# Kernel optimization log

Measured on AMD Instinct MI355X. Metric: run time of the kernel, lower is better.

## Reference

```python
import jax, jax.numpy as jnp
import numpy as np

N_NODES = 10000
N_EDGES = 160000
IN_DIM = 256
HEADS = 8
C0 = 32   # per-head out channels, layer 0 (256 // 8)
C1 = 32   # per-head out channels, layer 1 (= output_dim)
RANK = 8
LORA_SCALE = 32.0 / 8      # alpha / rank
ATT_RANK = 4               # rank // 2
ATT_SCALE = 32.0 / 4       # alpha / (rank // 2)
NEG_SLOPE = 0.2


def _gat_layer(x, src, dst, W, A, B, att_s, att_d, As, Bs, Ad, Bd, concat):
    """One LoRAGATConv layer (eval mode, dropout=0)."""
    N = x.shape[0]
    H, C = att_s.shape
    # LoRA-adapted projection: base + B(A x) * scaling -> [N, H, C]
    xp = (x @ W.T + ((x @ A.T) @ B.T) * LORA_SCALE).reshape(N, H, C)

    def att_score(base, Aa, Ba):
        # per-head base dot product + LoRA(out_channels -> 1) path -> [N, H]
        return jnp.einsum('nhc,hc->nh', xp, base) + ((xp @ Aa.T) @ Ba.T)[..., 0] * ATT_SCALE

    s_src = att_score(att_s, As, Bs)  # applied to x_i (destination), per original code
    s_dst = att_score(att_d, Ad, Bd)  # applied to x_j (source), per original code

    alpha = s_src[dst] + s_dst[src]              # [E, H]
    alpha = jax.nn.leaky_relu(alpha, NEG_SLOPE)
    # segment softmax over destination nodes (every node has a self-loop)
    m = jax.ops.segment_max(alpha, dst, num_segments=N)
    e = jnp.exp(alpha - m[dst])
    den = jax.ops.segment_sum(e, dst, num_segments=N)
    a = e / den[dst]                             # [E, H]

    msg = xp[src] * a[:, :, None]                # [E, H, C]
    out = jax.ops.segment_sum(msg, dst, num_segments=N)  # [N, H, C]
    return out.reshape(N, H * C) if concat else out.mean(axis=1)


def _forward(x, edge_index,
             W0, A0, B0, att_src0, att_dst0, Asrc0, Bsrc0, Adst0, Bdst0,
             W1, A1, B1, att_src1, att_dst1, Asrc1, Bsrc1, Adst1, Bdst1):
    N = x.shape[0]
    loops = jnp.arange(N, dtype=edge_index.dtype)
    ei = jnp.concatenate([edge_index, jnp.stack([loops, loops])], axis=1)
    src, dst = ei[0], ei[1]
    h = _gat_layer(x, src, dst, W0, A0, B0, att_src0, att_dst0, Asrc0, Bsrc0, Adst0, Bdst0, concat=True)
    h = jax.nn.elu(h)
    out = _gat_layer(h, src, dst, W1, A1, B1, att_src1, att_dst1, Asrc1, Bsrc1, Adst1, Bdst1, concat=False)
    return out


def setup_inputs() -> dict:
    key = jax.random.key(0)
    ks = jax.random.split(key, 24)
    s = 0.05
    inp = {
        'x': jax.random.normal(ks[0], (N_NODES, IN_DIM), dtype=jnp.float32),
        'edge_index': jax.random.randint(ks[1], (2, N_EDGES), 0, N_NODES, dtype=jnp.int64),
    }
    # layer 0: in 256 -> heads*C0 = 256
    inp['W0'] = jax.random.normal(ks[2], (HEADS * C0, IN_DIM), dtype=jnp.float32) * s
    inp['A0'] = jax.random.normal(ks[3], (RANK, IN_DIM), dtype=jnp.float32) * s
    inp['B0'] = jax.random.normal(ks[4], (HEADS * C0, RANK), dtype=jnp.float32) * s
    inp['att_src0'] = jax.random.normal(ks[5], (HEADS, C0), dtype=jnp.float32) * s
    inp['att_dst0'] = jax.random.normal(ks[6], (HEADS, C0), dtype=jnp.float32) * s
    inp['Asrc0'] = jax.random.normal(ks[7], (ATT_RANK, C0), dtype=jnp.float32) * s
    inp['Bsrc0'] = jax.random.normal(ks[8], (1, ATT_RANK), dtype=jnp.float32) * s
    inp['Adst0'] = jax.random.normal(ks[9], (ATT_RANK, C0), dtype=jnp.float32) * s
    inp['Bdst0'] = jax.random.normal(ks[10], (1, ATT_RANK), dtype=jnp.float32) * s
    # layer 1: in heads*C0 = 256 -> heads*C1 = 256 (head-averaged -> 32)
    D1 = HEADS * C0
    inp['W1'] = jax.random.normal(ks[11], (HEADS * C1, D1), dtype=jnp.float32) * s
    inp['A1'] = jax.random.normal(ks[12], (RANK, D1), dtype=jnp.float32) * s
    inp['B1'] = jax.random.normal(ks[13], (HEADS * C1, RANK), dtype=jnp.float32) * s
    inp['att_src1'] = jax.random.normal(ks[14], (HEADS, C1), dtype=jnp.float32) * s
    inp['att_dst1'] = jax.random.normal(ks[15], (HEADS, C1), dtype=jnp.float32) * s
    inp['Asrc1'] = jax.random.normal(ks[16], (ATT_RANK, C1), dtype=jnp.float32) * s
    inp['Bsrc1'] = jax.random.normal(ks[17], (1, ATT_RANK), dtype=jnp.float32) * s
    inp['Adst1'] = jax.random.normal(ks[18], (ATT_RANK, C1), dtype=jnp.float32) * s
    inp['Bdst1'] = jax.random.normal(ks[19], (1, ATT_RANK), dtype=jnp.float32) * s
    return inp


def reference(x, edge_index,
              W0, A0, B0, att_src0, att_dst0, Asrc0, Bsrc0, Adst0, Bdst0,
              W1, A1, B1, att_src1, att_dst1, Asrc1, Bsrc1, Adst1, Bdst1):
    return _forward(x, edge_index,
                    W0, A0, B0, att_src0, att_dst0, Asrc0, Bsrc0, Adst0, Bdst0,
                    W1, A1, B1, att_src1, att_dst1, Asrc1, Bsrc1, Adst1, Bdst1)
```

## Files before the change

### kernel.cpp

```cpp
#include <hip/hip_runtime.h>

#define LORA_SCALE 4.0f
#define ATT_SCALE 8.0f
#define NEG_SLOPE 0.2f
#define ELLW 64

typedef __attribute__((ext_vector_type(8))) short bf16x8;
typedef __attribute__((ext_vector_type(4))) float f32x4;
typedef unsigned short ushort_t;
typedef unsigned int uint_t;

__device__ inline ushort_t f2bf(float f) {
    uint_t u = __float_as_uint(f);
    u += 0x7fff + ((u >> 16) & 1);
    return (ushort_t)(u >> 16);
}
__device__ inline float bf2f(ushort_t h) {
    return __uint_as_float(((uint_t)h) << 16);
}
__device__ inline void split_bf(float f, ushort_t& h, ushort_t& l) {
    h = f2bf(f);
    l = f2bf(f - bf2f(h));
}

__global__ void prep_all(const float* __restrict__ W0, const float* __restrict__ A0,
                         const float* __restrict__ B0,
                         const float* __restrict__ att_s0, const float* __restrict__ att_d0,
                         const float* __restrict__ As0, const float* __restrict__ Bs0,
                         const float* __restrict__ Ad0, const float* __restrict__ Bd0,
                         const float* __restrict__ W1, const float* __restrict__ A1,
                         const float* __restrict__ B1,
                         const float* __restrict__ att_s1, const float* __restrict__ att_d1,
                         const float* __restrict__ As1, const float* __restrict__ Bs1,
                         const float* __restrict__ Ad1, const float* __restrict__ Bd1,
                         ushort_t* __restrict__ whi0, ushort_t* __restrict__ wlo0,
                         ushort_t* __restrict__ whi1, ushort_t* __restrict__ wlo1,
                         float* __restrict__ effS0, float* __restrict__ effD0,
                         float* __restrict__ effS1, float* __restrict__ effD1,
                         const float* __restrict__ x, ushort_t* __restrict__ xhi,
                         ushort_t* __restrict__ xlo,
                         const int* __restrict__ ei, int E_real, int E_total,
                         int* __restrict__ cnt, int* __restrict__ ell, int N)
{
    int b = blockIdx.x;
    int t = threadIdx.x;
    if (b < 512) {
        int layer = b >> 8;
        int i = (b & 255) * 256 + t;
        const float* W = layer ? W1 : W0;
        const float* A = layer ? A1 : A0;
        const float* B = layer ? B1 : B0;
        int r = i >> 8, c = i & 255;
        float acc = W[i];
        #pragma unroll
        for (int k = 0; k < 8; k++) acc += LORA_SCALE * B[r * 8 + k] * A[k * 256 + c];
        ushort_t h, l;
        split_bf(acc, h, l);
        if (layer) { whi1[i] = h; wlo1[i] = l; }
        else       { whi0[i] = h; wlo0[i] = l; }
        if (i < 256) {
            int c2 = i & 31;
            const float* as_ = layer ? att_s1 : att_s0;
            const float* ad_ = layer ? att_d1 : att_d0;
            const float* As = layer ? As1 : As0;
            const float* Bs = layer ? Bs1 : Bs0;
            const float* Ad = layer ? Ad1 : Ad0;
            const float* Bd = layer ? Bd1 : Bd0;
            float es = as_[i], ed = ad_[i];
            #pragma unroll
            for (int k = 0; k < 4; k++) {
                es += ATT_SCALE * Bs[k] * As[k * 32 + c2];
                ed += ATT_SCALE * Bd[k] * Ad[k * 32 + c2];
            }
            if (layer) { effS1[i] = es; effD1[i] = ed; }
            else       { effS0[i] = es; effD0[i] = ed; }
        }
        return;
    }
    int cb = b - 512;
    int convB = (N * 32 + 255) / 256;
    if (cb < convB) {
        int i = cb * 256 + t;
        if (i >= N * 32) return;
        float4 v0 = *(const float4*)(x + i * 8);
        float4 v1 = *(const float4*)(x + i * 8 + 4);
        ushort4 h0, l0, h1, l1;
        split_bf(v0.x, h0.x, l0.x);
        split_bf(v0.y, h0.y, l0.y);
        split_bf(v0.z, h0.z, l0.z);
        split_bf(v0.w, h0.w, l0.w);
        split_bf(v1.x, h1.x, l1.x);
        split_bf(v1.y, h1.y, l1.y);
        split_bf(v1.z, h1.z, l1.z);
        split_bf(v1.w, h1.w, l1.w);
        *(ushort4*)(xhi + i * 8) = h0;
        *(ushort4*)(xhi + i * 8 + 4) = h1;
        *(ushort4*)(xlo + i * 8) = l0;
        *(ushort4*)(xlo + i * 8 + 4) = l1;
        return;
    }
    int e = (cb - convB) * 256 + t;
    if (e >= E_total) return;
    int s, d;
    if (e < E_real) { s = ei[e]; d = ei[E_real + e]; }
    else            { s = d = e - E_real; }
    int pos = atomicAdd(&cnt[d], 1);
    if (pos < ELLW) ell[d * ELLW + pos] = s;
}

__global__ __launch_bounds__(512) void gemm_fused(
    const ushort_t* __restrict__ Ahi, const ushort_t* __restrict__ Alo,
    const ushort_t* __restrict__ Bhi, const ushort_t* __restrict__ Blo,
    const float* __restrict__ effS, const float* __restrict__ effD,
    ushort_t* __restrict__ Cb, float* __restrict__ ssrc, float* __restrict__ sdst, int M)
{
    __shared__ ushort_t sBh[16384];
    __shared__ ushort_t sBl[16384];
    const int K = 256;
    int tid = threadIdx.x;
    int n0 = blockIdx.x * 64;

    const ushort_t* srcH = Bhi + (size_t)n0 * K;
    const ushort_t* srcL = Blo + (size_t)n0 * K;
    #pragma unroll
    for (int c = 0; c < 4; c++) {
        int g  = c * 512 + tid;
        int rr = g >> 5;
        int ch = g & 31;
        int kblk = ch >> 2, quad = ch & 3;
        int tt = rr >> 4, l16r = rr & 15;
        int dst = (((tt * 8 + kblk) * 4 + quad) * 16 + l16r) * 8;
        *(bf16x8*)&sBh[dst] = *(const bf16x8*)(srcH + rr * K + ch * 8);
        *(bf16x8*)&sBl[dst] = *(const bf16x8*)(srcL + rr * K + ch * 8);
    }
    __syncthreads();

    int w = tid >> 6;
    int lane = tid & 63;
    int quad = lane >> 4;
    int l16 = lane & 15;
    int m0 = blockIdx.y * 128 + w * 16;
    int mr = m0 + l16; if (mr >= M) mr = M - 1;

    const ushort_t* ah = Ahi + mr * K + quad * 8;
    const ushort_t* al = Alo + mr * K + quad * 8;

    f32x4 acc[4] = {};
    #pragma unroll
    for (int kb = 0; kb < 8; kb++) {
        bf16x8 a_hi = *(const bf16x8*)(ah + kb * 32);
        bf16x8 a_lo = *(const bf16x8*)(al + kb * 32);
        #pragma unroll
        for (int t = 0; t < 4; t++) {
            int off = (((t * 8 + kb) * 4 + quad) * 16 + l16) * 8;
            bf16x8 b_hi = *(const bf16x8*)&sBh[off];
            bf16x8 b_lo = *(const bf16x8*)&sBl[off];
            acc[t] = __builtin_amdgcn_mfma_f32_16x16x32_bf16(a_hi, b_hi, acc[t], 0, 0, 0);
            acc[t] = __builtin_amdgcn_mfma_f32_16x16x32_bf16(a_hi, b_lo, acc[t], 0, 0, 0);
            acc[t] = __builtin_amdgcn_mfma_f32_16x16x32_bf16(a_lo, b_hi, acc[t], 0, 0, 0);
        }
    }

    #pragma unroll
    for (int t = 0; t < 4; t++) {
        #pragma unroll
        for (int r = 0; r < 4; r++) {
            int m = m0 + quad * 4 + r;
            if (m < M) Cb[m * 256 + n0 + t * 16 + l16] = f2bf(acc[t][r]);
        }
    }

    int h0 = n0 >> 5;
    float vs[2][4], vd[2][4];
    #pragma unroll
    for (int g = 0; g < 2; g++) {
        float e0s = effS[n0 + 32 * g + l16];
        float e1s = effS[n0 + 32 * g + 16 + l16];
        float e0d = effD[n0 + 32 * g + l16];
        float e1d = effD[n0 + 32 * g + 16 + l16];
        #pragma unroll
        for (int r = 0; r < 4; r++) {
            vs[g][r] = acc[2 * g][r] * e0s + acc[2 * g + 1][r] * e1s;
            vd[g][r] = acc[2 * g][r] * e0d + acc[2 * g + 1][r] * e1d;
        }
    }
    #pragma unroll
    for (int m = 1; m <= 8; m <<= 1) {
        #pragma unroll
        for (int g = 0; g < 2; g++)
            #pragma unroll
            for (int r = 0; r < 4; r++) {
                vs[g][r] += __shfl_xor(vs[g][r], m);
                vd[g][r] += __shfl_xor(vd[g][r], m);
            }
    }
    if (l16 == 0) {
        #pragma unroll
        for (int g = 0; g < 2; g++)
            #pragma unroll
            for (int r = 0; r < 4; r++) {
                int m = m0 + quad * 4 + r;
                if (m < M) {
                    ssrc[m * 8 + h0 + g] = vs[g][r];
                    sdst[m * 8 + h0 + g] = vd[g][r];
                }
            }
    }
}

__global__ __launch_bounds__(256) void ell_agg(const int* __restrict__ cnt,
                                               const int* __restrict__ ell,
                                               const ushort_t* __restrict__ xpb,
                                               const float* __restrict__ ssrc,
                                               const float* __restrict__ sdst,
                                               float* __restrict__ out,
                                               ushort_t* __restrict__ ohi,
                                               ushort_t* __restrict__ olo,
                                               int N, int mode)
{
    __shared__ int sidx[4][ELLW];
    int gid = blockIdx.x * blockDim.x + threadIdx.x;
    int d = gid >> 6;
    if (d >= N) return;
    int w = threadIdx.x >> 6;
    int lane = threadIdx.x & 63;
    int eo = lane >> 5;
    int l32 = lane & 31;
    int h = l32 >> 2;
    float ssrc_h = ssrc[d * 8 + h];
    int end = cnt[d]; if (end > ELLW) end = ELLW;
    const int* row = ell + d * ELLW;
    sidx[w][lane] = row[lane < end ? lane : 0];

    float acc[8] = {};
    float den = 0.f;
    for (int i = 0; i < end; i += 8) {
        int idx[4];
        #pragma unroll
        for (int p = 0; p < 4; p++) {
            int ii = i + 2 * p + eo;
            idx[p] = sidx[w][ii < end ? ii : 0];
        }
        float t4[4];
        #pragma unroll
        for (int p = 0; p < 4; p++) t4[p] = sdst[idx[p] * 8 + h];
        bf16x8 v[4];
        #pragma unroll
        for (int p = 0; p < 4; p++)
            v[p] = *(const bf16x8*)(xpb + idx[p] * 256 + l32 * 8);
        #pragma unroll
        for (int p = 0; p < 4; p++) {
            int ii = i + 2 * p + eo;
            float al = ssrc_h + t4[p];
            al = al > 0.f ? al : NEG_SLOPE * al;
            float wgt = (ii < end) ? __expf(al) : 0.f;
            den += wgt;
            #pragma unroll
            for (int j = 0; j < 8; j++)
                acc[j] += bf2f((ushort_t)v[p][j]) * wgt;
        }
    }
    #pragma unroll
    for (int j = 0; j < 8; j++) acc[j] += __shfl_xor(acc[j], 32);
    den += __shfl_xor(den, 32);
    float inv = 1.f / den;
    #pragma unroll
    for (int j = 0; j < 8; j++) acc[j] *= inv;

    if (mode == 2) {
        #pragma unroll
        for (int m = 4; m <= 16; m <<= 1)
            #pragma unroll
            for (int j = 0; j < 8; j++) acc[j] += __shfl_xor(acc[j], m);
        if (lane < 4) {
            float4 r0 = { acc[0] * 0.125f, acc[1] * 0.125f, acc[2] * 0.125f, acc[3] * 0.125f };
            float4 r1 = { acc[4] * 0.125f, acc[5] * 0.125f, acc[6] * 0.125f, acc[7] * 0.125f };
            *(float4*)(out + d * 32 + l32 * 8) = r0;
            *(float4*)(out + d * 32 + l32 * 8 + 4) = r1;
        }
        return;
    }
    #pragma unroll
    for (int j = 0; j < 8; j++)
        acc[j] = acc[j] > 0.f ? acc[j] : (__expf(acc[j]) - 1.f);
    if (eo == 0) {
        ushort_t hs[8], ls[8];
        #pragma unroll
        for (int j = 0; j < 8; j++) split_bf(acc[j], hs[j], ls[j]);
        *(ushort4*)(ohi + d * 256 + l32 * 8)     = *(ushort4*)&hs[0];
        *(ushort4*)(ohi + d * 256 + l32 * 8 + 4) = *(ushort4*)&hs[4];
        *(ushort4*)(olo + d * 256 + l32 * 8)     = *(ushort4*)&ls[0];
        *(ushort4*)(olo + d * 256 + l32 * 8 + 4) = *(ushort4*)&ls[4];
    }
}

extern "C" void kernel_launch(void* const* d_in, const int* in_sizes, int n_in,
                              void* d_out, int out_size, void* d_ws, size_t ws_size,
                              hipStream_t stream)
{
    const float* x  = (const float*)d_in[0];
    const int*   ei = (const int*)d_in[1];
    const float* W0 = (const float*)d_in[2];
    const float* A0 = (const float*)d_in[3];
    const float* B0 = (const float*)d_in[4];
    const float* att_s0 = (const float*)d_in[5];
    const float* att_d0 = (const float*)d_in[6];
    const float* As0 = (const float*)d_in[7];
    const float* Bs0 = (const float*)d_in[8];
    const float* Ad0 = (const float*)d_in[9];
    const float* Bd0 = (const float*)d_in[10];
    const float* W1 = (const float*)d_in[11];
    const float* A1 = (const float*)d_in[12];
    const float* B1 = (const float*)d_in[13];
    const float* att_s1 = (const float*)d_in[14];
    const float* att_d1 = (const float*)d_in[15];
    const float* As1 = (const float*)d_in[16];
    const float* Bs1 = (const float*)d_in[17];
    const float* Ad1 = (const float*)d_in[18];
    const float* Bd1 = (const float*)d_in[19];

    const int N = in_sizes[0] / 256;
    const int E_real = in_sizes[1] / 2;
    const int E_total = E_real + N;

    ushort_t* whi0 = (ushort_t*)d_ws;
    ushort_t* wlo0 = whi0 + 65536;
    ushort_t* whi1 = wlo0 + 65536;
    ushort_t* wlo1 = whi1 + 65536;
    ushort_t* xhi  = wlo1 + 65536;
    ushort_t* xlo  = xhi + 2560000;
    ushort_t* hbhi = xlo + 2560000;
    ushort_t* hblo = hbhi + 2560000;
    ushort_t* xpb  = hblo + 2560000;
    float* effS0 = (float*)(xpb + 2560000);
    float* effD0 = effS0 + 256;
    float* effS1 = effD0 + 256;
    float* effD1 = effS1 + 256;
    float* ssrc  = effD1 + 256;
    float* sdst  = ssrc + 80000;
    int* cnt = (int*)(sdst + 80000);
    int* ell = cnt + 10016;

    hipMemsetAsync(cnt, 0, (size_t)N * sizeof(int), stream);
    int convB = (N * 32 + 255) / 256;
    int fillB = (E_total + 255) / 256;
    prep_all<<<512 + convB + fillB, 256, 0, stream>>>(
        W0, A0, B0, att_s0, att_d0, As0, Bs0, Ad0, Bd0,
        W1, A1, B1, att_s1, att_d1, As1, Bs1, Ad1, Bd1,
        whi0, wlo0, whi1, wlo1, effS0, effD0, effS1, effD1,
        x, xhi, xlo, ei, E_real, E_total, cnt, ell, N);

    dim3 gg(4, (N + 127) / 128);
    int aggBlocks = (N * 64 + 255) / 256;

    gemm_fused<<<gg, 512, 0, stream>>>(xhi, xlo, whi0, wlo0, effS0, effD0, xpb, ssrc, sdst, N);
    ell_agg<<<aggBlocks, 256, 0, stream>>>(cnt, ell, xpb, ssrc, sdst,
                                           nullptr, hbhi, hblo, N, 1);

    gemm_fused<<<gg, 512, 0, stream>>>(hbhi, hblo, whi1, wlo1, effS1, effD1, xpb, ssrc, sdst, N);
    ell_agg<<<aggBlocks, 256, 0, stream>>>(cnt, ell, xpb, ssrc, sdst,
                                           (float*)d_out, nullptr, nullptr, N, 2);
}
```

Measured before the change: 167.6 us.

## Move ELL edge fill into first GEMM kernel and zero counters in prep kernel

Removes the separate memset launch by zeroing the per-node counters inside the prep kernel. Moves the edge-to-ELL scatter (atomicAdd per edge) out of the prep kernel into the tail of the first GEMM kernel via a templated grid-stride loop. This shortens the prep kernel and lets the atomic fill run alongside the GEMM blocks. The cost is extra work and registers in the layer-0 GEMM kernel. It also relies on kernel ordering so that cnt is zeroed before the GEMM runs.

Result: faster. 163.1 us (-2.7%).

```diff
diff --git a/kernel.cpp b/kernel.cpp
--- a/kernel.cpp
+++ b/kernel.cpp
@@ -39,8 +39,7 @@
                          float* __restrict__ effS1, float* __restrict__ effD1,
                          const float* __restrict__ x, ushort_t* __restrict__ xhi,
                          ushort_t* __restrict__ xlo,
-                         const int* __restrict__ ei, int E_real, int E_total,
-                         int* __restrict__ cnt, int* __restrict__ ell, int N)
+                         int* __restrict__ cnt, int N)
 {
     int b = blockIdx.x;
     int t = threadIdx.x;
@@ -99,20 +98,18 @@
         *(ushort4*)(xlo + i * 8 + 4) = l1;
         return;
     }
-    int e = (cb - convB) * 256 + t;
-    if (e >= E_total) return;
-    int s, d;
-    if (e < E_real) { s = ei[e]; d = ei[E_real + e]; }
-    else            { s = d = e - E_real; }
-    int pos = atomicAdd(&cnt[d], 1);
-    if (pos < ELLW) ell[d * ELLW + pos] = s;
-}
-
+    int i = (cb - convB) * 256 + t;
+    if (i < 10016) cnt[i] = 0;
+}
+
+template<int FILL>
 __global__ __launch_bounds__(512) void gemm_fused(
     const ushort_t* __restrict__ Ahi, const ushort_t* __restrict__ Alo,
     const ushort_t* __restrict__ Bhi, const ushort_t* __restrict__ Blo,
     const float* __restrict__ effS, const float* __restrict__ effD,
-    ushort_t* __restrict__ Cb, float* __restrict__ ssrc, float* __restrict__ sdst, int M)
+    ushort_t* __restrict__ Cb, float* __restrict__ ssrc, float* __restrict__ sdst,
+    const int* __restrict__ ei, int E_real, int E_total,
+    int* __restrict__ cnt, int* __restrict__ ell, int M)
 {
     __shared__ ushort_t sBh[16384];
     __shared__ ushort_t sBl[16384];
@@ -205,6 +202,18 @@
                     sdst[m * 8 + h0 + g] = vd[g][r];
                 }
             }
+    }
+
+    if (FILL) {
+        int stride = gridDim.x * gridDim.y * 512;
+        int base = (blockIdx.y * gridDim.x + blockIdx.x) * 512 + tid;
+        for (int e = base; e < E_total; e += stride) {
+            int s, d;
+            if (e < E_real) { s = ei[e]; d = ei[E_real + e]; }
+            else            { s = d = e - E_real; }
+            int pos = atomicAdd(&cnt[d], 1);
+            if (pos < ELLW) ell[d * ELLW + pos] = s;
+        }
     }
 }
 
@@ -237,27 +246,27 @@
     for (int i = 0; i < end; i += 8) {
         int idx[4];
         #pragma unroll
-        for (int p = 0; p < 4; p++) {
-            int ii = i + 2 * p + eo;
-            idx[p] = sidx[w][ii < end ? ii : 0];
+        for (int pp = 0; pp < 4; pp++) {
+            int ii = i + 2 * pp + eo;
+            idx[pp] = sidx[w][ii < end ? ii : 0];
         }
         float t4[4];
         #pragma unroll
-        for (int p = 0; p < 4; p++) t4[p] = sdst[idx[p] * 8 + h];
+        for (int pp = 0; pp < 4; pp++) t4[pp] = sdst[idx[pp] * 8 + h];
         bf16x8 v[4];
         #pragma unroll
-        for (int p = 0; p < 4; p++)
-            v[p] = *(const bf16x8*)(xpb + idx[p] * 256 + l32 * 8);
-        #pragma unroll
-        for (int p = 0; p < 4; p++) {
-            int ii = i + 2 * p + eo;
-            float al = ssrc_h + t4[p];
+        for (int pp = 0; pp < 4; pp++)
+            v[pp] = *(const bf16x8*)(xpb + idx[pp] * 256 + l32 * 8);
+        #pragma unroll
+        for (int pp = 0; pp < 4; pp++) {
+            int ii = i + 2 * pp + eo;
+            float al = ssrc_h + t4[pp];
             al = al > 0.f ? al : NEG_SLOPE * al;
             float wgt = (ii < end) ? __expf(al) : 0.f;
             den += wgt;
             #pragma unroll
             for (int j = 0; j < 8; j++)
-                acc[j] += bf2f((ushort_t)v[p][j]) * wgt;
+                acc[j] += bf2f((ushort_t)v[pp][j]) * wgt;
         }
     }
     #pragma unroll
@@ -341,23 +350,26 @@
     int* cnt = (int*)(sdst + 80000);
     int* ell = cnt + 10016;
 
-    hipMemsetAsync(cnt, 0, (size_t)N * sizeof(int), stream);
     int convB = (N * 32 + 255) / 256;
-    int fillB = (E_total + 255) / 256;
-    prep_all<<<512 + convB + fillB, 256, 0, stream>>>(
+    int cntB  = (10016 + 255) / 256;
+    prep_all<<<512 + convB + cntB, 256, 0, stream>>>(
         W0, A0, B0, att_s0, att_d0, As0, Bs0, Ad0, Bd0,
         W1, A1, B1, att_s1, att_d1, As1, Bs1, Ad1, Bd1,
         whi0, wlo0, whi1, wlo1, effS0, effD0, effS1, effD1,
-        x, xhi, xlo, ei, E_real, E_total, cnt, ell, N);
+        x, xhi, xlo, cnt, N);
 
     dim3 gg(4, (N + 127) / 128);
     int aggBlocks = (N * 64 + 255) / 256;
 
-    gemm_fused<<<gg, 512, 0, stream>>>(xhi, xlo, whi0, wlo0, effS0, effD0, xpb, ssrc, sdst, N);
+    gemm_fused<1><<<gg, 512, 0, stream>>>(xhi, xlo, whi0, wlo0, effS0, effD0,
+                                          xpb, ssrc, sdst,
+                                          ei, E_real, E_total, cnt, ell, N);
     ell_agg<<<aggBlocks, 256, 0, stream>>>(cnt, ell, xpb, ssrc, sdst,
                                            nullptr, hbhi, hblo, N, 1);
 
-    gemm_fused<<<gg, 512, 0, stream>>>(hbhi, hblo, whi1, wlo1, effS1, effD1, xpb, ssrc, sdst, N);
+    gemm_fused<0><<<gg, 512, 0, stream>>>(hbhi, hblo, whi1, wlo1, effS1, effD1,
+                                          xpb, ssrc, sdst,
+                                          nullptr, 0, 0, nullptr, nullptr, N);
     ell_agg<<<aggBlocks, 256, 0, stream>>>(cnt, ell, xpb, ssrc, sdst,
                                            (float*)d_out, nullptr, nullptr, N, 2);
 }
```
